# Optimization experiments

Measured on AMD Instinct MI355X. Metric: run time of the kernel, lower is better.

## Reference

```python
import jax, jax.numpy as jnp
import numpy as np

B, S, D = 4, 2048, 1024
H, DK = 16, 64
NEG = -1e9


def setup_inputs() -> dict:
    key = jax.random.key(0)
    ks = jax.random.split(key, 6)
    hidden_states = jax.random.normal(ks[0], (B, S, D), dtype=jnp.float32)
    # evidence-constrained mask: causal mask plus random evidence restriction
    causal = jnp.tril(jnp.ones((S, S), dtype=bool))
    evid = jax.random.bernoulli(ks[1], 0.7, (S, S))
    allowed = causal & (evid | jnp.eye(S, dtype=bool))  # diag always allowed
    attention_mask = jnp.where(allowed, 0.0, NEG).astype(jnp.float32)
    scale = 0.02
    Wq = jax.random.normal(ks[2], (H * DK, D), dtype=jnp.float32) * scale
    Wk = jax.random.normal(ks[3], (H * DK, D), dtype=jnp.float32) * scale
    Wv = jax.random.normal(ks[4], (H * DK, D), dtype=jnp.float32) * scale
    Wo = jax.random.normal(ks[5], (D, H * DK), dtype=jnp.float32) * scale
    return {"hidden_states": hidden_states, "attention_mask": attention_mask,
            "Wq": Wq, "Wk": Wk, "Wv": Wv, "Wo": Wo}


def reference(hidden_states, attention_mask, Wq, Wk, Wv, Wo):
    b, s, _ = hidden_states.shape
    # nn.Linear(bias=False): y = x @ W.T ; reshape to (B,H,S,DK)
    def proj(x, W):
        y = jnp.einsum('bsd,ed->bse', x, W)
        return y.reshape(b, s, H, DK).transpose(0, 2, 1, 3)
    q = proj(hidden_states, Wq)
    k = proj(hidden_states, Wk)
    v = proj(hidden_states, Wv)
    logits = jnp.einsum('bhqd,bhkd->bhqk', q, k) / jnp.sqrt(jnp.float32(DK))
    logits = logits + attention_mask[None, None, :, :]
    attn = jax.nn.softmax(logits, axis=-1)
    ctx = jnp.einsum('bhqk,bhkd->bhqd', attn, v)
    ctx = ctx.transpose(0, 2, 1, 3).reshape(b, s, H * DK)
    out = jnp.einsum('bse,de->bsd', ctx, Wo)
    return out
```

## Files before the change

### kernel.cpp

```cpp
#include <hip/hip_runtime.h>
#include <hip/hip_bf16.h>
#include <math.h>

#define B_  4
#define S_  2048
#define D_  1024
#define H_  16
#define DK_ 64
#define M_  (B_*S_)
#define E_  (H_*DK_)
#define LOG2E  1.4426950408889634f
#define QSCALE 0.18033688011112042f

typedef short  bf16x8 __attribute__((ext_vector_type(8)));
typedef float  f32x4  __attribute__((ext_vector_type(4)));
typedef unsigned short u16;
typedef unsigned int   u32;
typedef unsigned long long u64;

__device__ __forceinline__ u16 f2b(float x) {
    __hip_bfloat16 h = __float2bfloat16(x);
    return *(u16*)&h;
}

__device__ __forceinline__ u32 cvtpk(float lo, float hi) {
    u32 r;
    asm("v_cvt_pk_bf16_f32 %0, %1, %2" : "=v"(r) : "v"(lo), "v"(hi));
    return r;
}

__device__ __forceinline__ void async16(const u16* g, u16* l) {
    __builtin_amdgcn_global_load_lds(
        (const __attribute__((address_space(1))) unsigned int*)g,
        (__attribute__((address_space(3))) unsigned int*)l, 16, 0, 0);
}

#define XN8 (M_ * D_ / 8)
#define WN8 (E_ * D_ / 8)
__global__ __launch_bounds__(256)
void cvt_all(const float* __restrict__ X,
             const float* __restrict__ Wq, const float* __restrict__ Wk,
             const float* __restrict__ Wv, const float* __restrict__ Wo,
             u16* __restrict__ Xb,
             u16* __restrict__ Wqb, u16* __restrict__ Wkb,
             u16* __restrict__ Wvb, u16* __restrict__ Wob) {
    int idx = blockIdx.x * 256 + threadIdx.x;
    const float* s; u16* d; int off;
    if (idx < XN8) { s = X; d = Xb; off = idx; }
    else {
        int j = idx - XN8;
        int which = j / WN8; off = j - which * WN8;
        s = which == 0 ? Wq : which == 1 ? Wk : which == 2 ? Wv : Wo;
        d = which == 0 ? Wqb : which == 1 ? Wkb : which == 2 ? Wvb : Wob;
    }
    const float4* s4 = (const float4*)s;
    float4 a = s4[2 * off], b = s4[2 * off + 1];
    u16 o[8] = {f2b(a.x), f2b(a.y), f2b(a.z), f2b(a.w),
                f2b(b.x), f2b(b.y), f2b(b.z), f2b(b.w)};
    *(uint4*)(d + (size_t)8 * off) = *(const uint4*)o;
}

__global__ __launch_bounds__(256)
void maskcvt(const float* __restrict__ mask, u32* __restrict__ bits) {
    const int w   = threadIdx.x >> 6;
    const int lane = threadIdx.x & 63;
    const int row = blockIdx.x * 4 + w;
    const float* mr = mask + (size_t)row * S_;
    u64* br = (u64*)(bits + (size_t)row * (S_ / 32));
    #pragma unroll
    for (int i = 0; i < S_ / 64; i++) {
        float v = mr[i * 64 + lane];
        u64 bal = __ballot(v == 0.0f);
        if (lane == 0) br[i] = bal;
    }
}

__device__ __forceinline__ void gemm_core(
    const u16* __restrict__ Ag, const u16* __restrict__ Bg, int K,
    int bm, int bn, u16* As, u16* Bs, f32x4 (&acc)[4][4])
{
    const int tid  = threadIdx.x;
    const int w    = tid >> 6, lane = tid & 63;
    const int l15  = lane & 15, quad = lane >> 4;
    const int wm   = (w >> 1) * 64, wn = (w & 1) * 64;
    const int srow = lane >> 3;
    const int sg   = (lane & 7) ^ srow;
    const int sx   = l15 & 7;

    for (int k0 = 0; k0 < K; k0 += 64) {
        __syncthreads();
        #pragma unroll
        for (int i = 0; i < 4; i++) {
            const int row = w * 32 + i * 8 + srow;
            async16(Ag + (size_t)(bm + row) * K + k0 + sg * 8,
                    As + (size_t)(w * 32 + i * 8) * 64);
            async16(Bg + (size_t)(bn + row) * K + k0 + sg * 8,
                    Bs + (size_t)(w * 32 + i * 8) * 64);
        }
        __syncthreads();

        #pragma unroll
        for (int s = 0; s < 2; s++) {
            bf16x8 af[4], bf[4];
            #pragma unroll
            for (int i = 0; i < 4; i++)
                af[i] = *(const bf16x8*)(As + (size_t)(wm + i * 16 + l15) * 64
                                            + (((s * 4 + quad) ^ sx) * 8));
            #pragma unroll
            for (int j = 0; j < 4; j++)
                bf[j] = *(const bf16x8*)(Bs + (size_t)(wn + j * 16 + l15) * 64
                                            + (((s * 4 + quad) ^ sx) * 8));
            #pragma unroll
            for (int i = 0; i < 4; i++)
                #pragma unroll
                for (int j = 0; j < 4; j++)
                    acc[i][j] = __builtin_amdgcn_mfma_f32_16x16x32_bf16(af[i], bf[j], acc[i][j], 0, 0, 0);
        }
    }
}

__global__ __launch_bounds__(256)
void gemm_qkv(const u16* __restrict__ Xb,
              const u16* __restrict__ Wqb, const u16* __restrict__ Wkb,
              const u16* __restrict__ Wvb,
              u16* __restrict__ Qm, u16* __restrict__ Km, u16* __restrict__ Vt)
{
    __shared__ u16 As[128 * 64];
    __shared__ u16 Bs[128 * 64];
    const int bm    = blockIdx.x * 128;
    const int nb    = blockIdx.y;
    const int which = nb >> 3;
    const int col0  = (nb & 7) * 128;
    const u16* Bg = which == 0 ? Wqb : which == 1 ? Wkb : Wvb;

    f32x4 acc[4][4] = {};
    gemm_core(Xb, Bg, D_, bm, col0, As, Bs, acc);

    const int tid = threadIdx.x;
    const int w   = tid >> 6, lane = tid & 63;
    const int l15 = lane & 15, quad = lane >> 4;
    const int wm  = (w >> 1) * 64, wn = (w & 1) * 64;

    if (which == 2) {
        #pragma unroll
        for (int i = 0; i < 4; i++)
            #pragma unroll
            for (int j = 0; j < 4; j++) {
                int c    = col0 + wn + j * 16 + l15;
                int tok0 = bm + wm + i * 16 + quad * 4;
                int u    = tok0 & 63;
                int perm = (u & 32) | ((u & 12) << 1) | ((u & 16) >> 2);
                int tp   = (tok0 & (2047 & ~63)) | perm;
                u16 pk[4] = {f2b(acc[i][j][0]), f2b(acc[i][j][1]),
                             f2b(acc[i][j][2]), f2b(acc[i][j][3])};
                size_t idx = (((size_t)((tok0 >> 11) * E_ + c)) << 11) + tp;
                *(uint2*)(Vt + idx) = *(const uint2*)pk;
            }
    } else {
        u16* Cm = which == 0 ? Qm : Km;
        const float sc = which == 0 ? QSCALE : 1.0f;
        #pragma unroll
        for (int i = 0; i < 4; i++)
            #pragma unroll
            for (int j = 0; j < 4; j++)
                #pragma unroll
                for (int r = 0; r < 4; r++) {
                    int row = bm + wm + i * 16 + quad * 4 + r;
                    int c   = col0 + wn + j * 16 + l15;
                    Cm[(size_t)row * E_ + c] = f2b(acc[i][j][r] * sc);
                }
    }
}

__global__ __launch_bounds__(256)
void gemm_out(const u16* __restrict__ Cmx, const u16* __restrict__ Wob,
              float* __restrict__ out)
{
    __shared__ u16 As[128 * 64];
    __shared__ u16 Bs[128 * 64];
    const int bm = blockIdx.x * 128;
    const int bn = blockIdx.y * 128;

    f32x4 acc[4][4] = {};
    gemm_core(Cmx, Wob, E_, bm, bn, As, Bs, acc);

    const int tid = threadIdx.x;
    const int w   = tid >> 6, lane = tid & 63;
    const int l15 = lane & 15, quad = lane >> 4;
    const int wm  = (w >> 1) * 64, wn = (w & 1) * 64;
    #pragma unroll
    for (int i = 0; i < 4; i++)
        #pragma unroll
        for (int j = 0; j < 4; j++)
            #pragma unroll
            for (int r = 0; r < 4; r++)
                out[(size_t)(bm + wm + i * 16 + quad * 4 + r) * D_ + bn + wn + j * 16 + l15]
                    = acc[i][j][r];
}

__global__ __launch_bounds__(512)
void flash_attn(const u16* __restrict__ Q, const u16* __restrict__ Kc,
                const u16* __restrict__ Vt, const u32* __restrict__ bits,
                u16* __restrict__ ctx)
{
    const int bh  = blockIdx.x;
    const int qt  = (gridDim.y - 1) - blockIdx.y;
    const int b   = bh >> 4, h = bh & 15;
    const int tid = threadIdx.x;
    const int w   = tid >> 6, lane = tid & 63;
    const int l15 = lane & 15, quad = lane >> 4;
    const int q0  = qt * 128;
    const int nkt = 2 * qt + 2;

    __shared__ u16 Ks[2][64 * 64];
    __shared__ u16 Vs[2][64 * 64];

    const u16* qb = Q + ((size_t)(b * S_ + q0 + w * 16 + l15)) * E_ + h * DK_;
    bf16x8 qf0 = *(const bf16x8*)(qb + quad * 8);
    bf16x8 qf1 = *(const bf16x8*)(qb + 32 + quad * 8);

    f32x4 acc[4] = {};
    float lsum = 0.f;

    const int sr = lane >> 3;
    const int sg = (lane & 7) ^ sr;
    const int sx = l15 & 7;

    const u32* mrow = bits + (size_t)(q0 + w * 16 + l15) * (S_ / 32);
    const u16* kg = Kc + ((size_t)(b * S_ + w * 8 + sr)) * E_ + h * DK_ + sg * 8;
    const u16* vg = Vt + ((size_t)(bh * DK_ + w * 8 + sr)) * S_ + sg * 8;

    async16(kg, &Ks[0][w * 512]); kg += (size_t)64 * E_;
    async16(vg, &Vs[0][w * 512]); vg += 64;
    u64 mw_next = *(const u64*)mrow;

    int cur = 0;
    for (int kt = 0; kt < nkt; ++kt) {
        const int nxt = cur ^ 1;
        __syncthreads();
        u64 mw = mw_next;
        if (kt + 1 < nkt) {
            async16(kg, &Ks[nxt][w * 512]); kg += (size_t)64 * E_;
            async16(vg, &Vs[nxt][w * 512]); vg += 64;
            mw_next = *(const u64*)(mrow + ((kt + 1) << 1));
        }

        const u16* Kb = Ks[cur];
        f32x4 st[4] = {};
        #pragma unroll
        for (int t = 0; t < 4; t++) {
            bf16x8 kf0 = *(const bf16x8*)(Kb + (t * 16 + l15) * 64 + ((quad ^ sx) * 8));
            bf16x8 kf1 = *(const bf16x8*)(Kb + (t * 16 + l15) * 64 + (((4 + quad) ^ sx) * 8));
            st[t] = __builtin_amdgcn_mfma_f32_16x16x32_bf16(kf0, qf0, st[t], 0, 0, 0);
            st[t] = __builtin_amdgcn_mfma_f32_16x16x32_bf16(kf1, qf1, st[t], 0, 0, 0);
        }

        const u64 m2 = mw >> (quad * 4);
        const u32 mlo = (u32)m2, mhi = (u32)(m2 >> 32);
        const u32 nib[4] = { mlo & 0xF, (mlo >> 16) & 0xF,
                             mhi & 0xF, (mhi >> 16) & 0xF };
        #pragma unroll
        for (int t = 0; t < 4; t++) {
            st[t][0] = (nib[t] & 1) ? exp2f(st[t][0]) : 0.0f;
            st[t][1] = (nib[t] & 2) ? exp2f(st[t][1]) : 0.0f;
            st[t][2] = (nib[t] & 4) ? exp2f(st[t][2]) : 0.0f;
            st[t][3] = (nib[t] & 8) ? exp2f(st[t][3]) : 0.0f;
            lsum += (st[t][0] + st[t][1]) + (st[t][2] + st[t][3]);
        }

        const u16* Vb = Vs[cur];
        #pragma unroll
        for (int sb = 0; sb < 2; sb++) {
            union { u32 w4[4]; bf16x8 v; } pu;
            pu.w4[0] = cvtpk(st[2 * sb][0],     st[2 * sb][1]);
            pu.w4[1] = cvtpk(st[2 * sb][2],     st[2 * sb][3]);
            pu.w4[2] = cvtpk(st[2 * sb + 1][0], st[2 * sb + 1][1]);
            pu.w4[3] = cvtpk(st[2 * sb + 1][2], st[2 * sb + 1][3]);
            #pragma unroll
            for (int nt = 0; nt < 4; nt++) {
                bf16x8 vf = *(const bf16x8*)(Vb + (nt * 16 + l15) * 64
                                                + (((4 * sb + quad) ^ sx) * 8));
                acc[nt] = __builtin_amdgcn_mfma_f32_16x16x32_bf16(pu.v, vf, acc[nt], 0, 0, 0);
            }
        }
        cur = nxt;
    }

    lsum += __shfl_xor(lsum, 16, 64);
    lsum += __shfl_xor(lsum, 32, 64);
    float linv = 1.0f / lsum;
    float ir[4];
    #pragma unroll
    for (int r = 0; r < 4; r++) ir[r] = __shfl(linv, quad * 4 + r, 16);
    #pragma unroll
    for (int r = 0; r < 4; r++) {
        size_t orow = ((size_t)(b * S_ + q0 + w * 16 + quad * 4 + r)) * E_ + h * DK_;
        #pragma unroll
        for (int nt = 0; nt < 4; nt++)
            ctx[orow + nt * 16 + l15] = f2b(acc[nt][r] * ir[r]);
    }
}

extern "C" void kernel_launch(void* const* d_in, const int* in_sizes, int n_in,
                              void* d_out, int out_size, void* d_ws, size_t ws_size,
                              hipStream_t stream) {
    const float* X    = (const float*)d_in[0];
    const float* mask = (const float*)d_in[1];
    const float* Wq   = (const float*)d_in[2];
    const float* Wk   = (const float*)d_in[3];
    const float* Wv   = (const float*)d_in[4];
    const float* Wo   = (const float*)d_in[5];
    float* out = (float*)d_out;

    char* p = (char*)d_ws;
    u16* Qm  = (u16*)p; p += (size_t)M_ * E_ * 2;
    u16* Km  = (u16*)p; p += (size_t)M_ * E_ * 2;
    u16* Vt  = (u16*)p; p += (size_t)M_ * E_ * 2;
    u16* Wqb = (u16*)p; p += (size_t)E_ * D_ * 2;
    u16* Wkb = (u16*)p; p += (size_t)E_ * D_ * 2;
    u16* Wvb = (u16*)p; p += (size_t)E_ * D_ * 2;
    u16* Wob = (u16*)p; p += (size_t)D_ * E_ * 2;
    u32* Mb  = (u32*)p; p += (size_t)S_ * (S_ / 32) * 4;
    u16* Xb  = (u16*)p;
    u16* Cm  = Xb;

    cvt_all<<<(XN8 + 4 * WN8 + 255) / 256, 256, 0, stream>>>(
        X, Wq, Wk, Wv, Wo, Xb, Wqb, Wkb, Wvb, Wob);
    maskcvt<<<S_ / 4, 256, 0, stream>>>(mask, Mb);

    gemm_qkv<<<dim3(M_ / 128, 24), 256, 0, stream>>>(Xb, Wqb, Wkb, Wvb, Qm, Km, Vt);

    flash_attn<<<dim3(B_ * H_, S_ / 128), 512, 0, stream>>>(Qm, Km, Vt, Mb, Cm);

    gemm_out<<<dim3(M_ / 128, D_ / 128), 256, 0, stream>>>(Cm, Wob, out);
}
```

Measured before the change: 276.9 us.

## Process 32 query rows per wave in flash attention, MFMA row sums

Each wave now handles two 16-row query sub-tiles against every staged K/V tile, so the q-tile grows to 256 rows and each K/V fragment read from LDS is reused twice. The softmax denominator now comes from an MFMA against a ones vector, built from the bf16-rounded probabilities, instead of scalar adds and cross-lane shuffles. Query tiles are reordered so the heaviest causal blocks launch first and the rest follow in ascending order. The costs are half as many blocks (fewer waves to fill the machine), more registers per thread, and coarser causal granularity that does extra masked work near the diagonal.

Result: slower. 288.1 us (+4.0%).

```diff
diff --git a/kernel.cpp b/kernel.cpp
--- a/kernel.cpp
+++ b/kernel.cpp
@@ -198,106 +198,131 @@
                     = acc[i][j][r];
 }
 
-__global__ __launch_bounds__(512)
+__global__ __launch_bounds__(512, 4)
 void flash_attn(const u16* __restrict__ Q, const u16* __restrict__ Kc,
                 const u16* __restrict__ Vt, const u32* __restrict__ bits,
                 u16* __restrict__ ctx)
 {
     const int bh  = blockIdx.x;
-    const int qt  = (gridDim.y - 1) - blockIdx.y;
+    const int y   = blockIdx.y;
+    const int qt  = (y < 4) ? (7 - y) : (y - 4);
     const int b   = bh >> 4, h = bh & 15;
     const int tid = threadIdx.x;
     const int w   = tid >> 6, lane = tid & 63;
     const int l15 = lane & 15, quad = lane >> 4;
-    const int q0  = qt * 128;
-    const int nkt = 2 * qt + 2;
+    const int q0  = qt * 256;
+    const int nkt = 4 * qt + 4;
 
     __shared__ u16 Ks[2][64 * 64];
     __shared__ u16 Vs[2][64 * 64];
 
-    const u16* qb = Q + ((size_t)(b * S_ + q0 + w * 16 + l15)) * E_ + h * DK_;
-    bf16x8 qf0 = *(const bf16x8*)(qb + quad * 8);
-    bf16x8 qf1 = *(const bf16x8*)(qb + 32 + quad * 8);
-
-    f32x4 acc[4] = {};
-    float lsum = 0.f;
+    const u16* qbA = Q + ((size_t)(b * S_ + q0 + w * 32 + l15)) * E_ + h * DK_;
+    bf16x8 qfA0 = *(const bf16x8*)(qbA + quad * 8);
+    bf16x8 qfA1 = *(const bf16x8*)(qbA + 32 + quad * 8);
+    const u16* qbB = qbA + (size_t)16 * E_;
+    bf16x8 qfB0 = *(const bf16x8*)(qbB + quad * 8);
+    bf16x8 qfB1 = *(const bf16x8*)(qbB + 32 + quad * 8);
+
+    f32x4 accA[4] = {}, accB[4] = {};
+    f32x4 accLA = {}, accLB = {};
 
     const int sr = lane >> 3;
     const int sg = (lane & 7) ^ sr;
     const int sx = l15 & 7;
 
-    const u32* mrow = bits + (size_t)(q0 + w * 16 + l15) * (S_ / 32);
+    const u32* mrowA = bits + (size_t)(q0 + w * 32 + l15) * (S_ / 32);
+    const u32* mrowB = mrowA + 16 * (S_ / 32);
     const u16* kg = Kc + ((size_t)(b * S_ + w * 8 + sr)) * E_ + h * DK_ + sg * 8;
     const u16* vg = Vt + ((size_t)(bh * DK_ + w * 8 + sr)) * S_ + sg * 8;
 
     async16(kg, &Ks[0][w * 512]); kg += (size_t)64 * E_;
     async16(vg, &Vs[0][w * 512]); vg += 64;
-    u64 mw_next = *(const u64*)mrow;
+    u64 mwAn = *(const u64*)mrowA;
+    u64 mwBn = *(const u64*)mrowB;
+
+    union { u32 w4[4]; bf16x8 v; } ones;
+    ones.w4[0] = ones.w4[1] = ones.w4[2] = ones.w4[3] = 0x3F803F80u;
 
     int cur = 0;
     for (int kt = 0; kt < nkt; ++kt) {
         const int nxt = cur ^ 1;
         __syncthreads();
-        u64 mw = mw_next;
+        u64 mwA = mwAn, mwB = mwBn;
         if (kt + 1 < nkt) {
             async16(kg, &Ks[nxt][w * 512]); kg += (size_t)64 * E_;
             async16(vg, &Vs[nxt][w * 512]); vg += 64;
-            mw_next = *(const u64*)(mrow + ((kt + 1) << 1));
+            mwAn = *(const u64*)(mrowA + ((kt + 1) << 1));
+            mwBn = *(const u64*)(mrowB + ((kt + 1) << 1));
         }
 
         const u16* Kb = Ks[cur];
-        f32x4 st[4] = {};
-        #pragma unroll
-        for (int t = 0; t < 4; t++) {
-            bf16x8 kf0 = *(const bf16x8*)(Kb + (t * 16 + l15) * 64 + ((quad ^ sx) * 8));
-            bf16x8 kf1 = *(const bf16x8*)(Kb + (t * 16 + l15) * 64 + (((4 + quad) ^ sx) * 8));
-            st[t] = __builtin_amdgcn_mfma_f32_16x16x32_bf16(kf0, qf0, st[t], 0, 0, 0);
-            st[t] = __builtin_amdgcn_mfma_f32_16x16x32_bf16(kf1, qf1, st[t], 0, 0, 0);
-        }
-
-        const u64 m2 = mw >> (quad * 4);
-        const u32 mlo = (u32)m2, mhi = (u32)(m2 >> 32);
-        const u32 nib[4] = { mlo & 0xF, (mlo >> 16) & 0xF,
-                             mhi & 0xF, (mhi >> 16) & 0xF };
-        #pragma unroll
-        for (int t = 0; t < 4; t++) {
-            st[t][0] = (nib[t] & 1) ? exp2f(st[t][0]) : 0.0f;
-            st[t][1] = (nib[t] & 2) ? exp2f(st[t][1]) : 0.0f;
-            st[t][2] = (nib[t] & 4) ? exp2f(st[t][2]) : 0.0f;
-            st[t][3] = (nib[t] & 8) ? exp2f(st[t][3]) : 0.0f;
-            lsum += (st[t][0] + st[t][1]) + (st[t][2] + st[t][3]);
-        }
-
         const u16* Vb = Vs[cur];
+
         #pragma unroll
         for (int sb = 0; sb < 2; sb++) {
-            union { u32 w4[4]; bf16x8 v; } pu;
-            pu.w4[0] = cvtpk(st[2 * sb][0],     st[2 * sb][1]);
-            pu.w4[1] = cvtpk(st[2 * sb][2],     st[2 * sb][3]);
-            pu.w4[2] = cvtpk(st[2 * sb + 1][0], st[2 * sb + 1][1]);
-            pu.w4[3] = cvtpk(st[2 * sb + 1][2], st[2 * sb + 1][3]);
+            f32x4 stA[2] = {}, stB[2] = {};
+            #pragma unroll
+            for (int tt = 0; tt < 2; tt++) {
+                const int t = 2 * sb + tt;
+                bf16x8 kf0 = *(const bf16x8*)(Kb + (t * 16 + l15) * 64 + ((quad ^ sx) * 8));
+                bf16x8 kf1 = *(const bf16x8*)(Kb + (t * 16 + l15) * 64 + (((4 + quad) ^ sx) * 8));
+                stA[tt] = __builtin_amdgcn_mfma_f32_16x16x32_bf16(kf0, qfA0, stA[tt], 0, 0, 0);
+                stA[tt] = __builtin_amdgcn_mfma_f32_16x16x32_bf16(kf1, qfA1, stA[tt], 0, 0, 0);
+                stB[tt] = __builtin_amdgcn_mfma_f32_16x16x32_bf16(kf0, qfB0, stB[tt], 0, 0, 0);
+                stB[tt] = __builtin_amdgcn_mfma_f32_16x16x32_bf16(kf1, qfB1, stB[tt], 0, 0, 0);
+            }
+
+            const u64 sA = mwA >> (quad * 4 + sb * 32);
+            const u64 sB = mwB >> (quad * 4 + sb * 32);
+            #pragma unroll
+            for (int tt = 0; tt < 2; tt++) {
+                const u32 nA = (u32)(sA >> (tt * 16)) & 0xF;
+                const u32 nB = (u32)(sB >> (tt * 16)) & 0xF;
+                stA[tt][0] = (nA & 1) ? exp2f(stA[tt][0]) : 0.0f;
+                stA[tt][1] = (nA & 2) ? exp2f(stA[tt][1]) : 0.0f;
+                stA[tt][2] = (nA & 4) ? exp2f(stA[tt][2]) : 0.0f;
+                stA[tt][3] = (nA & 8) ? exp2f(stA[tt][3]) : 0.0f;
+                stB[tt][0] = (nB & 1) ? exp2f(stB[tt][0]) : 0.0f;
+                stB[tt][1] = (nB & 2) ? exp2f(stB[tt][1]) : 0.0f;
+                stB[tt][2] = (nB & 4) ? exp2f(stB[tt][2]) : 0.0f;
+                stB[tt][3] = (nB & 8) ? exp2f(stB[tt][3]) : 0.0f;
+            }
+
+            union { u32 w4[4]; bf16x8 v; } puA, puB;
+            puA.w4[0] = cvtpk(stA[0][0], stA[0][1]);
+            puA.w4[1] = cvtpk(stA[0][2], stA[0][3]);
+            puA.w4[2] = cvtpk(stA[1][0], stA[1][1]);
+            puA.w4[3] = cvtpk(stA[1][2], stA[1][3]);
+            puB.w4[0] = cvtpk(stB[0][0], stB[0][1]);
+            puB.w4[1] = cvtpk(stB[0][2], stB[0][3]);
+            puB.w4[2] = cvtpk(stB[1][0], stB[1][1]);
+            puB.w4[3] = cvtpk(stB[1][2], stB[1][3]);
+
+            accLA = __builtin_amdgcn_mfma_f32_16x16x32_bf16(puA.v, ones.v, accLA, 0, 0, 0);
+            accLB = __builtin_amdgcn_mfma_f32_16x16x32_bf16(puB.v, ones.v, accLB, 0, 0, 0);
+
             #pragma unroll
             for (int nt = 0; nt < 4; nt++) {
                 bf16x8 vf = *(const bf16x8*)(Vb + (nt * 16 + l15) * 64
                                                 + (((4 * sb + quad) ^ sx) * 8));
-                acc[nt] = __builtin_amdgcn_mfma_f32_16x16x32_bf16(pu.v, vf, acc[nt], 0, 0, 0);
+                accA[nt] = __builtin_amdgcn_mfma_f32_16x16x32_bf16(puA.v, vf, accA[nt], 0, 0, 0);
+                accB[nt] = __builtin_amdgcn_mfma_f32_16x16x32_bf16(puB.v, vf, accB[nt], 0, 0, 0);
             }
         }
         cur = nxt;
     }
 
-    lsum += __shfl_xor(lsum, 16, 64);
-    lsum += __shfl_xor(lsum, 32, 64);
-    float linv = 1.0f / lsum;
-    float ir[4];
-    #pragma unroll
-    for (int r = 0; r < 4; r++) ir[r] = __shfl(linv, quad * 4 + r, 16);
     #pragma unroll
     for (int r = 0; r < 4; r++) {
-        size_t orow = ((size_t)(b * S_ + q0 + w * 16 + quad * 4 + r)) * E_ + h * DK_;
-        #pragma unroll
-        for (int nt = 0; nt < 4; nt++)
-            ctx[orow + nt * 16 + l15] = f2b(acc[nt][r] * ir[r]);
+        float irA = 1.0f / accLA[r];
+        float irB = 1.0f / accLB[r];
+        size_t oA = ((size_t)(b * S_ + q0 + w * 32 + quad * 4 + r)) * E_ + h * DK_;
+        size_t oB = oA + (size_t)16 * E_;
+        #pragma unroll
+        for (int nt = 0; nt < 4; nt++) {
+            ctx[oA + nt * 16 + l15] = f2b(accA[nt][r] * irA);
+            ctx[oB + nt * 16 + l15] = f2b(accB[nt][r] * irB);
+        }
     }
 }
 
@@ -330,7 +355,7 @@
 
     gemm_qkv<<<dim3(M_ / 128, 24), 256, 0, stream>>>(Xb, Wqb, Wkb, Wvb, Qm, Km, Vt);
 
-    flash_attn<<<dim3(B_ * H_, S_ / 128), 512, 0, stream>>>(Qm, Km, Vt, Mb, Cm);
+    flash_attn<<<dim3(B_ * H_, S_ / 256), 512, 0, stream>>>(Qm, Km, Vt, Mb, Cm);
 
     gemm_out<<<dim3(M_ / 128, D_ / 128), 256, 0, stream>>>(Cm, Wob, out);
 }
```
